# Optimization experiments

Measured on AMD Instinct MI355X. Metric: run time of the kernel, lower is better.

The kernel has to match this reference:

```python
import jax, jax.numpy as jnp
import numpy as np

B, C, D = 512, 100000, 512
MARGIN = 0.5  # ArcFace-style additive angular margin


def setup_inputs() -> dict:
    key = jax.random.key(0)
    k1, k2, k3 = jax.random.split(key, 3)
    embeddings = jax.random.normal(k1, (B, D), dtype=jnp.float32)
    labels = jax.random.randint(k2, (B,), 0, C, dtype=jnp.int32)
    weight = 0.01 * jax.random.normal(k3, (C, D), dtype=jnp.float32)  # torch.normal(0, 0.01, (C, D))
    return {"embeddings": embeddings, "labels": labels, "weight": weight}


def _l2_normalize(x, eps=1e-12):
    return x / jnp.maximum(jnp.linalg.norm(x, axis=-1, keepdims=True), eps)


def reference(embeddings, labels, weight):
    cos_m = jnp.cos(MARGIN)
    sin_m = jnp.sin(MARGIN)

    e = _l2_normalize(embeddings)          # (B, D)
    w = _l2_normalize(weight)              # (C, D)
    logits = jnp.clip(jnp.einsum('bd,cd->bc', e, w), -1.0, 1.0)  # (B, C) cosines

    bsz, ncls = logits.shape
    rows = jnp.arange(bsz)
    cos_t = logits[rows, labels]                                   # (B,) cos(theta_y)
    sin_t = jnp.sqrt(jnp.clip(1.0 - cos_t * cos_t, 0.0, None))     # sin(theta_y)
    cos_tm = cos_t * cos_m - sin_t * sin_m                         # cos(theta_y + m)
    sin_tm = sin_t * cos_m + cos_t * sin_m                         # sin(theta_y + m)

    # non-target class indices per row, ascending, skipping the target: (B, C-1)
    base = jnp.arange(ncls - 1)[None, :]
    nt_idx = base + (base >= labels[:, None]).astype(base.dtype)

    # margin_softmax: logits2 = cos(theta_j) - cos(theta_y + m) over non-target j
    nt_logits = jnp.take_along_axis(logits, nt_idx, axis=1)       # (B, C-1)
    logits2 = nt_logits - cos_tm[:, None]

    # no_grad block: weight_m is unit-norm point at angle theta_y+m from e,
    # so ||w_j - w_m||^2 = 2 - 2 <w_j, w_m>  (avoids materializing (B, C, D)).
    w_y = w[labels]                                                # (B, D)
    w_m = (-sin_m * e + sin_tm[:, None] * w_y) / sin_t[:, None]    # (B, D), unit norm
    sim = jnp.einsum('bd,cd->bc', w_m, w)                          # (B, C)
    nt_sim = jnp.take_along_axis(sim, nt_idx, axis=1)              # (B, C-1)
    diff_weight_norm = jax.lax.stop_gradient(
        jnp.sqrt(jnp.clip(2.0 - 2.0 * nt_sim, 0.0, None)))         # (B, C-1)

    e_logits = jnp.sum(jnp.exp(logits2 / diff_weight_norm), axis=1)  # (B,)
    return jnp.mean(jnp.log1p(e_logits))
```

## Files before the change

### kernel.cpp

```cpp
#include <hip/hip_runtime.h>
#include <hip/hip_fp8.h>
#include <math.h>

#define B_SZ 512
#define C_SZ 100000
#define D_SZ 512

#define BN 128
#define NTILES 782
#define MT 8
#define NBLK (NTILES * MT)
#define KSTEPS 8
#define DEPTH 3

typedef __attribute__((ext_vector_type(4))) float f32x4;
typedef __attribute__((ext_vector_type(16))) float f32x16;
typedef __attribute__((ext_vector_type(4))) int i32x4;
typedef __attribute__((ext_vector_type(8))) int i32x8;

#define UNITY_SCALE 0x7F7F7F7F

__device__ __forceinline__ void gload_lds16(const void* gptr, void* lptr) {
  __builtin_amdgcn_global_load_lds(
      (const __attribute__((address_space(1))) void*)gptr,
      (__attribute__((address_space(3))) void*)lptr,
      16, 0, 0);
}

__device__ __forceinline__ unsigned char f2fp8(float x) {
  __hip_fp8_e4m3 h(x);
  return (unsigned char)h.__x;
}
__device__ __forceinline__ float fp82f(unsigned int u) {
  __hip_fp8_e4m3 h;
  h.__x = (unsigned char)u;
  return (float)h;
}
__device__ __forceinline__ unsigned int pack4f8(float a, float b, float c, float d) {
  return (unsigned int)f2fp8(a) | ((unsigned int)f2fp8(b) << 8) |
         ((unsigned int)f2fp8(c) << 16) | ((unsigned int)f2fp8(d) << 24);
}

__device__ __forceinline__ i32x8 ld_frag(const unsigned char* base, int frag, int l) {
  i32x4 lo = *(const i32x4*)(base + frag * 2048 + l * 16);
  i32x4 hg = *(const i32x4*)(base + frag * 2048 + 1024 + l * 16);
  return __builtin_shufflevector(lo, hg, 0, 1, 2, 3, 4, 5, 6, 7);
}
__device__ __forceinline__ i32x8 ld_a(const unsigned char* p) {
  i32x4 lo = *(const i32x4*)(p);
  i32x4 hg = *(const i32x4*)(p + 1024);
  return __builtin_shufflevector(lo, hg, 0, 1, 2, 3, 4, 5, 6, 7);
}

__global__ __launch_bounds__(256) void k_norm_w(const float* __restrict__ w,
                                                unsigned char* __restrict__ w8) {
  const int row = blockIdx.x * 4 + (threadIdx.x >> 6);
  const int lane = threadIdx.x & 63;
  const float4* wr = (const float4*)(w + (size_t)row * D_SZ);
  float4 v0 = wr[lane];
  float4 v1 = wr[64 + lane];
  float ss = v0.x*v0.x + v0.y*v0.y + v0.z*v0.z + v0.w*v0.w
           + v1.x*v1.x + v1.y*v1.y + v1.z*v1.z + v1.w*v1.w;
  #pragma unroll
  for (int o = 32; o; o >>= 1) ss += __shfl_xor(ss, o, 64);
  const float rn = __builtin_amdgcn_rsqf(fmaxf(ss, 1e-24f));
  unsigned int* out = (unsigned int*)(w8 + (size_t)row * D_SZ);
  out[lane] = pack4f8(v0.x * rn, v0.y * rn, v0.z * rn, v0.w * rn);
  out[64 + lane] = pack4f8(v1.x * rn, v1.y * rn, v1.z * rn, v1.w * rn);
}

__global__ __launch_bounds__(64) void k_prep(const float* __restrict__ e,
                                             const int* __restrict__ labels,
                                             const unsigned char* __restrict__ w8,
                                             unsigned char* __restrict__ A8f,
                                             float4* __restrict__ params) {
  const int b = blockIdx.x;
  const int lane = threadIdx.x;
  const float4* er = (const float4*)(e + (size_t)b * D_SZ);
  float4 v0 = er[lane], v1 = er[64 + lane];
  float ss = v0.x*v0.x + v0.y*v0.y + v0.z*v0.z + v0.w*v0.w
           + v1.x*v1.x + v1.y*v1.y + v1.z*v1.z + v1.w*v1.w;
  #pragma unroll
  for (int o = 32; o; o >>= 1) ss += __shfl_xor(ss, o, 64);
  const float rn = __builtin_amdgcn_rsqf(fmaxf(ss, 1e-24f));
  v0.x *= rn; v0.y *= rn; v0.z *= rn; v0.w *= rn;
  v1.x *= rn; v1.y *= rn; v1.z *= rn; v1.w *= rn;

  const unsigned int ue0 = pack4f8(v0.x, v0.y, v0.z, v0.w);
  const unsigned int ue1 = pack4f8(v1.x, v1.y, v1.z, v1.w);

  const int lab = labels[b];
  const unsigned int* wr = (const unsigned int*)(w8 + (size_t)lab * D_SZ);
  const unsigned int w0 = wr[lane], w1 = wr[64 + lane];

  const int re = 2 * b;
  const int frag = re >> 5;
  const int rife = re & 31;
  const int wk = (4 * lane) & 63;
  const int ks = lane >> 4;
  const int sbits = (((wk >> 5) & 1) << 5) | (((wk >> 4) & 1) << 6);
  const int byteo = wk & 15;
  unsigned char* fb = A8f + (size_t)frag * 16384;
  unsigned char* pe = fb + (rife | sbits) * 16 + byteo;
  unsigned char* pw = fb + ((rife + 1) | sbits) * 16 + byteo;
  *(unsigned int*)(pe + ks * 2048) = ue0;
  *(unsigned int*)(pe + (ks + 4) * 2048) = ue1;
  *(unsigned int*)(pw + ks * 2048) = w0;
  *(unsigned int*)(pw + (ks + 4) * 2048) = w1;

  float d = v0.x * fp82f(w0 & 255) + v0.y * fp82f((w0 >> 8) & 255)
          + v0.z * fp82f((w0 >> 16) & 255) + v0.w * fp82f(w0 >> 24)
          + v1.x * fp82f(w1 & 255) + v1.y * fp82f((w1 >> 8) & 255)
          + v1.z * fp82f((w1 >> 16) & 255) + v1.w * fp82f(w1 >> 24);
  #pragma unroll
  for (int o = 32; o; o >>= 1) d += __shfl_xor(d, o, 64);

  if (lane == 0) {
    const float cos_m = 0.877582561890372716f;
    const float sin_m = 0.479425538604203000f;
    float cos_t = fminf(fmaxf(d, -1.0f), 1.0f);
    float sin_t = sqrtf(fmaxf(1.0f - cos_t * cos_t, 0.0f));
    float cos_tm = cos_t * cos_m - sin_t * sin_m;
    float sin_tm = sin_t * cos_m + cos_t * sin_m;
    float inv_st = 1.0f / fmaxf(sin_t, 1e-20f);
    params[b] = make_float4(cos_tm, sin_m * inv_st, sin_tm * inv_st, 0.0f);
  }
}

__device__ __forceinline__ float termf(float de, float dwy, float4 p, bool kill) {
  float c = fminf(fmaxf(de, -1.0f), 1.0f);
  float s = p.z * dwy - p.y * de;
  float x = fmaxf(fmaf(-2.0f, s, 2.0f), 1e-20f);
  float t = (c - p.x) * __builtin_amdgcn_rsqf(x);
  float r = __expf(t);
  return kill ? 0.0f : r;
}

__global__ __launch_bounds__(512, 6) void k_gemm(const unsigned char* __restrict__ A8f,
                                                 const unsigned char* __restrict__ W8,
                                                 const float4* __restrict__ params,
                                                 const int* __restrict__ labels,
                                                 float* __restrict__ part) {
  __shared__ __align__(32) unsigned char Bt[DEPTH][BN * 64];
  __shared__ float ered[64];
  __shared__ float4 pl[64];
  __shared__ int ll[64];

  const int bid = blockIdx.x;
  const int p = (bid & 7) * (NBLK / 8) + (bid >> 3);
  const int nt = p >> 3, mt = p & 7;
  const int t = threadIdx.x;
  const int w = t >> 6, l = t & 63;
  const int n0 = nt * BN;
  const int b0 = mt * 64;

  if (t < 64) {
    ered[t] = 0.0f;
    pl[t] = params[b0 + t];
    ll[t] = labels[b0 + t];
  }

  const int kpart = ((t >> 5) & 1) * 32 + ((t >> 6) & 1) * 16;
  int brow_s = n0 + (t >> 7) * 32 + (t & 31);
  if (brow_s >= C_SZ) brow_s = C_SZ - 1;
  const int boffs = brow_s * D_SZ + kpart;

  const unsigned char* afb =
      A8f + (size_t)(mt * 4 + (w & 3)) * 16384 + l * 16;

  f32x16 accA = {}, accB = {};
  const int fA = w & 3;
  const int fB0 = (w >> 2) * 2;
  const int hi = l >> 5;

#define STAGE(d, ts)                                                        \
  gload_lds16(W8 + (size_t)(boffs + (ts) * 64), (void*)(Bt[d] + t * 16))

  STAGE(0, 0);
  STAGE(1, 1);
  STAGE(2, 2);
  asm volatile("s_waitcnt vmcnt(2) lgkmcnt(0)" ::: "memory");
  __builtin_amdgcn_s_barrier();

  #pragma unroll
  for (int s = 0; s < KSTEPS; ++s) {
    const int d = s % DEPTH;
    i32x8 av = ld_a(afb + s * 2048);
    i32x8 bv = ld_frag(Bt[d], fB0, l);
    __builtin_amdgcn_s_setprio(1);
    accA = __builtin_amdgcn_mfma_scale_f32_32x32x64_f8f6f4(
        av, bv, accA, 0, 0, 0, UNITY_SCALE, 0, UNITY_SCALE);
    bv = ld_frag(Bt[d], fB0 + 1, l);
    accB = __builtin_amdgcn_mfma_scale_f32_32x32x64_f8f6f4(
        av, bv, accB, 0, 0, 0, UNITY_SCALE, 0, UNITY_SCALE);
    __builtin_amdgcn_s_setprio(0);
    if (s < KSTEPS - 1) {
      if (s < KSTEPS - 2)
        asm volatile("s_waitcnt vmcnt(1)" ::: "memory");
      else
        asm volatile("s_waitcnt vmcnt(0)" ::: "memory");
      __builtin_amdgcn_s_barrier();
      if (s + 3 < KSTEPS)
        STAGE(d, s + 3);
    }
  }
#undef STAGE

  #pragma unroll
  for (int rp = 0; rp < 8; ++rp) {
    const int r = 2 * rp;
    const int lb = fA * 16 + (rp & 1) + 4 * (rp >> 1) + 2 * hi;
    float4 pp = pl[lb];
    int lab = ll[lb];
    int j0 = n0 + fB0 * 32 + (l & 31);
    int j1 = j0 + 32;
    float s = termf(accA[r], accA[r + 1], pp, (j0 >= C_SZ) || (j0 == lab))
            + termf(accB[r], accB[r + 1], pp, (j1 >= C_SZ) || (j1 == lab));
    #pragma unroll
    for (int o = 1; o < 32; o <<= 1) s += __shfl_xor(s, o, 64);
    if ((l & 31) == 0) atomicAdd(&ered[lb], s);
  }
  __syncthreads();
  if (t < 64) part[(size_t)(b0 + t) * NTILES + nt] = ered[t];
}

__global__ __launch_bounds__(256) void k_rowsum(const float* __restrict__ part,
                                                float* __restrict__ rowsum) {
  const int b = blockIdx.x;
  float s = 0.0f;
  for (int i = threadIdx.x; i < NTILES; i += 256) s += part[(size_t)b * NTILES + i];
  #pragma unroll
  for (int o = 32; o; o >>= 1) s += __shfl_xor(s, o, 64);
  __shared__ float red[4];
  if ((threadIdx.x & 63) == 0) red[threadIdx.x >> 6] = s;
  __syncthreads();
  if (threadIdx.x == 0)
    rowsum[b] = log1pf(red[0] + red[1] + red[2] + red[3]);
}

__global__ __launch_bounds__(512) void k_final(const float* __restrict__ rowsum,
                                               float* __restrict__ out) {
  const int b = threadIdx.x;
  float v = rowsum[b];
  __shared__ float red[512];
  red[b] = v;
  __syncthreads();
  #pragma unroll
  for (int o = 256; o; o >>= 1) {
    if (b < o) red[b] += red[b + o];
    __syncthreads();
  }
  if (b == 0) out[0] = red[0] / (float)B_SZ;
}

extern "C" void kernel_launch(void* const* d_in, const int* in_sizes, int n_in,
                              void* d_out, int out_size, void* d_ws, size_t ws_size,
                              hipStream_t stream) {
  const float* emb = (const float*)d_in[0];
  const int* labels = (const int*)d_in[1];
  const float* w = (const float*)d_in[2];

  char* ws = (char*)d_ws;
  unsigned char* w8 = (unsigned char*)ws;
  size_t off = (size_t)C_SZ * D_SZ;
  unsigned char* A8f = (unsigned char*)(ws + off);
  off += (size_t)2 * B_SZ * D_SZ;
  float4* params = (float4*)(ws + off);
  off += (size_t)B_SZ * 16;
  float* part = (float*)(ws + off);
  off += (size_t)B_SZ * NTILES * 4;
  float* rowsum = (float*)(ws + off);
  off += (size_t)B_SZ * 4;

  k_norm_w<<<dim3(C_SZ / 4), dim3(256), 0, stream>>>(w, w8);
  k_prep<<<dim3(B_SZ), dim3(64), 0, stream>>>(emb, labels, w8, A8f, params);
  k_gemm<<<dim3(NBLK), dim3(512), 0, stream>>>(A8f, w8, params, labels, part);
  k_rowsum<<<dim3(B_SZ), dim3(256), 0, stream>>>(part, rowsum);
  k_final<<<dim3(1), dim3(512), 0, stream>>>(rowsum, (float*)d_out);
}
```

Baseline: 135.6 us.

## Retile FP8 GEMM to 64-column blocks with four A fragments per wave

Each block now handles 64 weight columns across half the batch with 256 threads. Each wave holds eight 32x32 accumulators and reuses every B fragment read from LDS across four A fragments, instead of one. The epilogue drops the shared-memory atomic reduction and writes per-row partial sums straight to global memory. The partial-sum buffer and the row-sum kernel change to the finer 64-column tiling. This raises MFMA density per LDS read but increases register pressure, doubles the partial writes, and re-reads params and labels from global memory in the epilogue.

```diff
diff --git a/kernel.cpp b/kernel.cpp
--- a/kernel.cpp
+++ b/kernel.cpp
@@ -6,10 +6,9 @@
 #define C_SZ 100000
 #define D_SZ 512
 
-#define BN 128
-#define NTILES 782
-#define MT 8
-#define NBLK (NTILES * MT)
+#define BN 64
+#define NT64 1564
+#define NBLK (NT64 * 2)
 #define KSTEPS 8
 #define DEPTH 3
 
@@ -136,29 +135,19 @@
   return kill ? 0.0f : r;
 }
 
-__global__ __launch_bounds__(512, 6) void k_gemm(const unsigned char* __restrict__ A8f,
+__global__ __launch_bounds__(256, 2) void k_gemm(const unsigned char* __restrict__ A8f,
                                                  const unsigned char* __restrict__ W8,
                                                  const float4* __restrict__ params,
                                                  const int* __restrict__ labels,
                                                  float* __restrict__ part) {
   __shared__ __align__(32) unsigned char Bt[DEPTH][BN * 64];
-  __shared__ float ered[64];
-  __shared__ float4 pl[64];
-  __shared__ int ll[64];
 
   const int bid = blockIdx.x;
   const int p = (bid & 7) * (NBLK / 8) + (bid >> 3);
-  const int nt = p >> 3, mt = p & 7;
+  const int nt = p >> 1, mhalf = p & 1;
   const int t = threadIdx.x;
   const int w = t >> 6, l = t & 63;
   const int n0 = nt * BN;
-  const int b0 = mt * 64;
-
-  if (t < 64) {
-    ered[t] = 0.0f;
-    pl[t] = params[b0 + t];
-    ll[t] = labels[b0 + t];
-  }
 
   const int kpart = ((t >> 5) & 1) * 32 + ((t >> 6) & 1) * 16;
   int brow_s = n0 + (t >> 7) * 32 + (t & 31);
@@ -166,12 +155,12 @@
   const int boffs = brow_s * D_SZ + kpart;
 
   const unsigned char* afb =
-      A8f + (size_t)(mt * 4 + (w & 3)) * 16384 + l * 16;
-
-  f32x16 accA = {}, accB = {};
-  const int fA = w & 3;
-  const int fB0 = (w >> 2) * 2;
+      A8f + (size_t)(mhalf * 16 + w * 4) * 16384 + l * 16;
+
+  f32x16 c00 = {}, c01 = {}, c10 = {}, c11 = {};
+  f32x16 c20 = {}, c21 = {}, c30 = {}, c31 = {};
   const int hi = l >> 5;
+  const int col = l & 31;
 
 #define STAGE(d, ts)                                                        \
   gload_lds16(W8 + (size_t)(boffs + (ts) * 64), (void*)(Bt[d] + t * 16))
@@ -185,14 +174,31 @@
   #pragma unroll
   for (int s = 0; s < KSTEPS; ++s) {
     const int d = s % DEPTH;
-    i32x8 av = ld_a(afb + s * 2048);
-    i32x8 bv = ld_frag(Bt[d], fB0, l);
+    i32x8 av0 = ld_a(afb + 0 * 16384 + s * 2048);
+    i32x8 av1 = ld_a(afb + 1 * 16384 + s * 2048);
+    i32x8 av2 = ld_a(afb + 2 * 16384 + s * 2048);
+    i32x8 av3 = ld_a(afb + 3 * 16384 + s * 2048);
+    i32x8 bv = ld_frag(Bt[d], 0, l);
     __builtin_amdgcn_s_setprio(1);
-    accA = __builtin_amdgcn_mfma_scale_f32_32x32x64_f8f6f4(
-        av, bv, accA, 0, 0, 0, UNITY_SCALE, 0, UNITY_SCALE);
-    bv = ld_frag(Bt[d], fB0 + 1, l);
-    accB = __builtin_amdgcn_mfma_scale_f32_32x32x64_f8f6f4(
-        av, bv, accB, 0, 0, 0, UNITY_SCALE, 0, UNITY_SCALE);
+    c00 = __builtin_amdgcn_mfma_scale_f32_32x32x64_f8f6f4(
+        av0, bv, c00, 0, 0, 0, UNITY_SCALE, 0, UNITY_SCALE);
+    c10 = __builtin_amdgcn_mfma_scale_f32_32x32x64_f8f6f4(
+        av1, bv, c10, 0, 0, 0, UNITY_SCALE, 0, UNITY_SCALE);
+    c20 = __builtin_amdgcn_mfma_scale_f32_32x32x64_f8f6f4(
+        av2, bv, c20, 0, 0, 0, UNITY_SCALE, 0, UNITY_SCALE);
+    c30 = __builtin_amdgcn_mfma_scale_f32_32x32x64_f8f6f4(
+        av3, bv, c30, 0, 0, 0, UNITY_SCALE, 0, UNITY_SCALE);
+    __builtin_amdgcn_s_setprio(0);
+    bv = ld_frag(Bt[d], 1, l);
+    __builtin_amdgcn_s_setprio(1);
+    c01 = __builtin_amdgcn_mfma_scale_f32_32x32x64_f8f6f4(
+        av0, bv, c01, 0, 0, 0, UNITY_SCALE, 0, UNITY_SCALE);
+    c11 = __builtin_amdgcn_mfma_scale_f32_32x32x64_f8f6f4(
+        av1, bv, c11, 0, 0, 0, UNITY_SCALE, 0, UNITY_SCALE);
+    c21 = __builtin_amdgcn_mfma_scale_f32_32x32x64_f8f6f4(
+        av2, bv, c21, 0, 0, 0, UNITY_SCALE, 0, UNITY_SCALE);
+    c31 = __builtin_amdgcn_mfma_scale_f32_32x32x64_f8f6f4(
+        av3, bv, c31, 0, 0, 0, UNITY_SCALE, 0, UNITY_SCALE);
     __builtin_amdgcn_s_setprio(0);
     if (s < KSTEPS - 1) {
       if (s < KSTEPS - 2)
@@ -206,29 +212,36 @@
   }
 #undef STAGE
 
-  #pragma unroll
-  for (int rp = 0; rp < 8; ++rp) {
-    const int r = 2 * rp;
-    const int lb = fA * 16 + (rp & 1) + 4 * (rp >> 1) + 2 * hi;
-    float4 pp = pl[lb];
-    int lab = ll[lb];
-    int j0 = n0 + fB0 * 32 + (l & 31);
-    int j1 = j0 + 32;
-    float s = termf(accA[r], accA[r + 1], pp, (j0 >= C_SZ) || (j0 == lab))
-            + termf(accB[r], accB[r + 1], pp, (j1 >= C_SZ) || (j1 == lab));
-    #pragma unroll
-    for (int o = 1; o < 32; o <<= 1) s += __shfl_xor(s, o, 64);
-    if ((l & 31) == 0) atomicAdd(&ered[lb], s);
-  }
-  __syncthreads();
-  if (t < 64) part[(size_t)(b0 + t) * NTILES + nt] = ered[t];
+#define EPI(CM0, CM1, MF)                                                   \
+  do {                                                                      \
+    _Pragma("unroll")                                                       \
+    for (int rp = 0; rp < 8; ++rp) {                                        \
+      const int r = 2 * rp;                                                 \
+      const int rowk = (rp & 1) + 4 * (rp >> 1) + 2 * hi;                   \
+      const int gb = (mhalf * 16 + w * 4 + (MF)) * 16 + rowk;               \
+      float4 pp = params[gb];                                               \
+      int lab = labels[gb];                                                 \
+      int j0 = n0 + col, j1 = j0 + 32;                                      \
+      float sv = termf(CM0[r], CM0[r + 1], pp, (j0 >= C_SZ) || (j0 == lab)) \
+               + termf(CM1[r], CM1[r + 1], pp, (j1 >= C_SZ) || (j1 == lab));\
+      _Pragma("unroll")                                                     \
+      for (int o = 1; o < 32; o <<= 1) sv += __shfl_xor(sv, o, 64);         \
+      if (col == 0) part[(size_t)gb * NT64 + nt] = sv;                      \
+    }                                                                       \
+  } while (0)
+
+  EPI(c00, c01, 0);
+  EPI(c10, c11, 1);
+  EPI(c20, c21, 2);
+  EPI(c30, c31, 3);
+#undef EPI
 }
 
 __global__ __launch_bounds__(256) void k_rowsum(const float* __restrict__ part,
                                                 float* __restrict__ rowsum) {
   const int b = blockIdx.x;
   float s = 0.0f;
-  for (int i = threadIdx.x; i < NTILES; i += 256) s += part[(size_t)b * NTILES + i];
+  for (int i = threadIdx.x; i < NT64; i += 256) s += part[(size_t)b * NT64 + i];
   #pragma unroll
   for (int o = 32; o; o >>= 1) s += __shfl_xor(s, o, 64);
   __shared__ float red[4];
@@ -268,13 +281,13 @@
   float4* params = (float4*)(ws + off);
   off += (size_t)B_SZ * 16;
   float* part = (float*)(ws + off);
-  off += (size_t)B_SZ * NTILES * 4;
+  off += (size_t)B_SZ * NT64 * 4;
   float* rowsum = (float*)(ws + off);
   off += (size_t)B_SZ * 4;
 
   k_norm_w<<<dim3(C_SZ / 4), dim3(256), 0, stream>>>(w, w8);
   k_prep<<<dim3(B_SZ), dim3(64), 0, stream>>>(emb, labels, w8, A8f, params);
-  k_gemm<<<dim3(NBLK), dim3(512), 0, stream>>>(A8f, w8, params, labels, part);
+  k_gemm<<<dim3(NBLK), dim3(256), 0, stream>>>(A8f, w8, params, labels, part);
   k_rowsum<<<dim3(B_SZ), dim3(256), 0, stream>>>(part, rowsum);
   k_final<<<dim3(1), dim3(512), 0, stream>>>(rowsum, (float*)d_out);
 }
```

Result: slower. 315.7 us (+132.8%).
